# Kernel tuning notes

Measured on AMD Instinct MI355X. Metric: run time of the kernel, lower is better.

The kernel has to match this reference:

```python
import jax, jax.numpy as jnp
import numpy as np

B, T, U = 8, 200, 50
D_ENC, D_DEC, D_FUSION, VOCAB = 512, 512, 640, 1024


def setup_inputs() -> dict:
    key = jax.random.key(0)
    ks = jax.random.split(key, 11)
    s = lambda d: 1.0 / np.sqrt(d)
    return {
        "encoder_out": jax.random.normal(ks[0], (B, T, D_ENC), jnp.float32),
        "decoder_out": jax.random.normal(ks[1], (B, U, D_DEC), jnp.float32),
        "ot_decoder_feature": jax.random.normal(ks[2], (B, T, D_DEC), jnp.float32),
        "W_enc": jax.random.uniform(ks[3], (D_ENC, D_FUSION), jnp.float32, -s(D_ENC), s(D_ENC)),
        "b_enc": jax.random.uniform(ks[4], (D_FUSION,), jnp.float32, -s(D_ENC), s(D_ENC)),
        "W_ot": jax.random.uniform(ks[5], (D_DEC, D_FUSION), jnp.float32, -s(D_DEC), s(D_DEC)),
        "b_ot": jax.random.uniform(ks[6], (D_FUSION,), jnp.float32, -s(D_DEC), s(D_DEC)),
        "W_dec": jax.random.uniform(ks[7], (D_DEC, D_FUSION), jnp.float32, -s(D_DEC), s(D_DEC)),
        "b_dec": jax.random.uniform(ks[8], (D_FUSION,), jnp.float32, -s(D_DEC), s(D_DEC)),
        "W_out": jax.random.uniform(ks[9], (D_FUSION, VOCAB), jnp.float32, -s(D_FUSION), s(D_FUSION)),
        "b_out": jax.random.uniform(ks[10], (VOCAB,), jnp.float32, -s(D_FUSION), s(D_FUSION)),
    }


def reference(encoder_out, decoder_out, ot_decoder_feature,
              W_enc, b_enc, W_ot, b_ot, W_dec, b_dec, W_out, b_out):
    # proj_enc + proj_ot_dec: both [B, T, d_fusion]
    fused = (jnp.einsum('bte,ef->btf', encoder_out, W_enc) + b_enc
             + jnp.einsum('btd,df->btf', ot_decoder_feature, W_ot) + b_ot)
    proj_dec = jnp.einsum('bud,df->buf', decoder_out, W_dec) + b_dec  # [B, U, d_fusion]
    # broadcast add over T x U, tanh, then final projection to vocab
    joint = jnp.tanh(fused[:, :, None, :] + proj_dec[:, None, :, :])  # [B, T, U, d_fusion]
    logits = jnp.einsum('btuf,fv->btuv', joint, W_out) + b_out  # [B, T, U, vocab]
    return logits
```

## Files before the change

### kernel.cpp

```cpp
#include <hip/hip_runtime.h>
#include <math.h>

typedef __bf16 bf16_t;
typedef __bf16 bf16x8 __attribute__((ext_vector_type(8)));
typedef float f32x4 __attribute__((ext_vector_type(4)));
typedef int i32x4 __attribute__((ext_vector_type(4)));
typedef int i32x2 __attribute__((ext_vector_type(2)));

#define SW_SCALE 0.03952847075f

#define GLOAD_LDS16(g, l)                                                      \
  __builtin_amdgcn_global_load_lds(                                            \
      (const __attribute__((address_space(1))) void*)(g),                      \
      (__attribute__((address_space(3))) void*)(l), 16, 0, 0)

__global__ __launch_bounds__(256) void prep_kernel(
    const float* __restrict__ enc, const float* __restrict__ dec,
    const float* __restrict__ ot, const float* __restrict__ W_enc,
    const float* __restrict__ W_ot, const float* __restrict__ W_dec,
    const float* __restrict__ W_out, bf16_t* __restrict__ Acat,
    bf16_t* __restrict__ Dec, bf16_t* __restrict__ WcatT,
    bf16_t* __restrict__ WdecT, signed char* __restrict__ WoutT8) {
  __shared__ float T[32][33];
  const int tid = threadIdx.x;
  const int b = blockIdx.x;

  if (b < 900) {
    const int idx8 = (b * 256 + tid) * 8;
    const int N0 = 1600 * 1024;
    if (idx8 < N0) {
      const int r = idx8 >> 10, c = idx8 & 1023;
      const float* src = (c < 512) ? enc + (r << 9) + c : ot + (r << 9) + c - 512;
      f32x4 v0 = *(const f32x4*)src;
      f32x4 v1 = *(const f32x4*)(src + 4);
      bf16x8 o;
#pragma unroll
      for (int e = 0; e < 4; ++e) {
        o[e] = (bf16_t)v0[e];
        o[e + 4] = (bf16_t)v1[e];
      }
      *(bf16x8*)(Acat + idx8) = o;
    } else {
      const int j = idx8 - N0;
      if (j < 400 * 512) {
        f32x4 v0 = *(const f32x4*)(dec + j);
        f32x4 v1 = *(const f32x4*)(dec + j + 4);
        bf16x8 o;
#pragma unroll
        for (int e = 0; e < 4; ++e) {
          o[e] = (bf16_t)v0[e];
          o[e + 4] = (bf16_t)v1[e];
        }
        *(bf16x8*)(Dec + j) = o;
      }
    }
    return;
  }

  const int tx = tid & 31, ty = tid >> 5;
  if (b < 1540) {
    const int b2 = b - 900;
    const int kt = b2 / 20, ft = b2 - kt * 20;
    const int k0 = kt * 32, f0 = ft * 32;
#pragma unroll
    for (int j = 0; j < 4; ++j) {
      const int kk = k0 + ty + j * 8;
      T[ty + j * 8][tx] = (kk < 512) ? W_enc[kk * 640 + f0 + tx]
                                     : W_ot[(kk - 512) * 640 + f0 + tx];
    }
    __syncthreads();
#pragma unroll
    for (int j = 0; j < 4; ++j) {
      const int ff = f0 + ty + j * 8;
      WcatT[ff * 1024 + k0 + tx] = (bf16_t)T[tx][ty + j * 8];
    }
    return;
  }
  if (b < 1860) {
    const int b2 = b - 1540;
    const int kt = b2 / 20, ft = b2 - kt * 20;
    const int k0 = kt * 32, f0 = ft * 32;
#pragma unroll
    for (int j = 0; j < 4; ++j)
      T[ty + j * 8][tx] = W_dec[(k0 + ty + j * 8) * 640 + f0 + tx];
    __syncthreads();
#pragma unroll
    for (int j = 0; j < 4; ++j) {
      const int ff = f0 + ty + j * 8;
      WdecT[ff * 512 + k0 + tx] = (bf16_t)T[tx][ty + j * 8];
    }
    return;
  }
  {
    const int b2 = b - 1860;
    const int vt = b2 / 20, ft = b2 - vt * 20;
    const int v0 = vt * 32, f0 = ft * 32;
#pragma unroll
    for (int j = 0; j < 4; ++j)
      T[ty + j * 8][tx] = W_out[(f0 + ty + j * 8) * 1024 + v0 + tx];
    __syncthreads();
#pragma unroll
    for (int j = 0; j < 4; ++j) {
      const int vv = v0 + ty + j * 8;
      float w = T[tx][ty + j * 8] * (127.0f / SW_SCALE);
      w = fminf(fmaxf(w, -127.0f), 127.0f);
      WoutT8[(size_t)vv * 640 + f0 + tx] = (signed char)__float2int_rn(w);
    }
  }
}

__global__ __launch_bounds__(256) void gemm_tanh_kernel(
    const bf16_t* __restrict__ A, const bf16_t* __restrict__ Bt,
    const float* __restrict__ bias1, const float* __restrict__ bias2,
    float* __restrict__ out, int M, int K) {
  __shared__ __align__(16) unsigned char L[2][16384];
  const int tid = threadIdx.x;
  const int wid = tid >> 6, l = tid & 63;
  const int wm = wid >> 1, wn = wid & 1;
  const int r0 = blockIdx.y * 64, n0 = blockIdx.x * 64;

  const int sperm = ((l & 3) ^ ((l >> 3) & 3)) * 8;
  int ra0 = r0 + wm * 32 + (l >> 2);
  if (ra0 > M - 1) ra0 = M - 1;
  int ra1 = r0 + wm * 32 + 16 + (l >> 2);
  if (ra1 > M - 1) ra1 = M - 1;
  const bf16_t* gA0 = A + (size_t)ra0 * K + sperm;
  const bf16_t* gA1 = A + (size_t)ra1 * K + sperm;
  const bf16_t* gB0 = Bt + (size_t)(n0 + wn * 32 + (l >> 2)) * K + sperm;
  const bf16_t* gB1 = gB0 + (size_t)16 * K;
  const int wb = wid * 4096;

  const int lr = l & 15, kg = l >> 4;
  const int swz = (kg ^ ((lr >> 1) & 3)) << 4;
  const int aO = wb + lr * 64 + swz;
  const int bO = wb + 2048 + lr * 64 + swz;

#define ST1_STAGE(t, buf)                                                      \
  {                                                                            \
    GLOAD_LDS16(gA0 + (t) * 32, L[buf] + wb);                                  \
    GLOAD_LDS16(gA1 + (t) * 32, L[buf] + wb + 1024);                           \
    GLOAD_LDS16(gB0 + (t) * 32, L[buf] + wb + 2048);                           \
    GLOAD_LDS16(gB1 + (t) * 32, L[buf] + wb + 3072);                           \
  }

  f32x4 acc[2][2] = {};
  const int steps = K >> 5;
  ST1_STAGE(0, 0);
#pragma unroll 1
  for (int ks = 0; ks < steps; ++ks) {
    const int cur = ks & 1, nxt = cur ^ 1;
    if (ks < steps - 1) ST1_STAGE(ks + 1, nxt);
    __builtin_amdgcn_sched_barrier(0);
    if (ks < steps - 1) {
      asm volatile("s_waitcnt vmcnt(4)" ::: "memory");
    } else {
      asm volatile("s_waitcnt vmcnt(0)" ::: "memory");
    }
    __builtin_amdgcn_sched_barrier(0);
    bf16x8 af[2], bfr[2];
#pragma unroll
    for (int a = 0; a < 2; ++a)
      af[a] = *(const bf16x8*)(L[cur] + aO + a * 1024);
#pragma unroll
    for (int b = 0; b < 2; ++b)
      bfr[b] = *(const bf16x8*)(L[cur] + bO + b * 1024);
#pragma unroll
    for (int a = 0; a < 2; ++a)
#pragma unroll
      for (int b = 0; b < 2; ++b)
        acc[a][b] = __builtin_amdgcn_mfma_f32_16x16x32_bf16(af[a], bfr[b],
                                                            acc[a][b], 0, 0, 0);
  }
#undef ST1_STAGE

#pragma unroll
  for (int a = 0; a < 2; ++a)
#pragma unroll
    for (int b = 0; b < 2; ++b) {
      int col = n0 + wn * 32 + b * 16 + lr;
      float bv = bias1[col] + (bias2 ? bias2[col] : 0.0f);
#pragma unroll
      for (int j = 0; j < 4; ++j) {
        int rg = r0 + wm * 32 + a * 16 + kg * 4 + j;
        if (rg < M) out[(size_t)rg * 640 + col] = tanhf(acc[a][b][j] + bv);
      }
    }
}

__global__ __launch_bounds__(256) void materialize8_kernel(
    const float* __restrict__ ta,
    const float* __restrict__ tb,
    signed char* __restrict__ A8) {
  const int idx = blockIdx.x * 256 + threadIdx.x;
  const int row = idx / 80;
  const int c8 = idx - row * 80;
  const int frow = row / 50;
  const int bidx = row / 10000;
  const int u = row - frow * 50;
  const float* tap = ta + (size_t)frow * 640 + c8 * 8;
  const float* tbp = tb + (size_t)(bidx * 50 + u) * 640 + c8 * 8;
  f32x4 xa0 = *(const f32x4*)tap, xa1 = *(const f32x4*)(tap + 4);
  f32x4 xb0 = *(const f32x4*)tbp, xb1 = *(const f32x4*)(tbp + 4);
  int q[8];
#pragma unroll
  for (int e = 0; e < 4; ++e) {
    float d0 = fmaxf(1.0f + xa0[e] * xb0[e], 1e-6f);
    q[e] = __float2int_rn((xa0[e] + xb0[e]) * __builtin_amdgcn_rcpf(d0) * 127.0f);
    float d1 = fmaxf(1.0f + xa1[e] * xb1[e], 1e-6f);
    q[e + 4] =
        __float2int_rn((xa1[e] + xb1[e]) * __builtin_amdgcn_rcpf(d1) * 127.0f);
  }
  i32x2 pk;
  pk[0] = (q[0] & 255) | ((q[1] & 255) << 8) | ((q[2] & 255) << 16) | (q[3] << 24);
  pk[1] = (q[4] & 255) | ((q[5] & 255) << 8) | ((q[6] & 255) << 16) | (q[7] << 24);
  *(i32x2*)(A8 + (size_t)row * 656 + c8 * 8) = pk;
}

__global__ __launch_bounds__(512, 4) void joint_gemm_kernel(
    const signed char* __restrict__ A8,
    const signed char* __restrict__ W8,
    const float* __restrict__ b_out,
    float* __restrict__ out) {
  __shared__ __align__(16) signed char Al[2][21504];
  __shared__ __align__(16) float Tr[8][32 * 20];
  const int tid = threadIdx.x;
  const int w = tid >> 6, l = tid & 63;
  const int lr = l & 15, kg = l >> 4;

  const int orig = blockIdx.x;
  const int mg = (orig & 7) + 8 * (orig >> 6);
  const int strip = (orig >> 3) & 7;
  if (mg >= 313) return;
  const int c0w = strip * 128 + w * 16;

  i32x4 Bf[10];
  const signed char* gW = W8 + (size_t)(c0w + lr) * 640 + kg * 16;
#pragma unroll
  for (int t = 0; t < 10; ++t) Bf[t] = *(const i32x4*)(gW + t * 64);
  const float bv = b_out[c0w + lr];

  const int i0 = w * 3;
  const int ni = (i0 < 21) ? ((i0 + 3 <= 21) ? 3 : 21 - i0) : 0;
  const size_t mbase = (size_t)mg * 256 * 656;

#define JSTAGE(c, buf)                                                         \
  {                                                                            \
    const signed char* s_ = A8 + mbase + (size_t)(c) * (32 * 656);             \
    for (int k_ = 0; k_ < ni; ++k_) {                                          \
      const int i_ = i0 + k_;                                                  \
      const int off_ = (i_ == 20) ? 19968 : i_ * 1024;                         \
      GLOAD_LDS16(s_ + off_ + l * 16, Al[buf] + off_);                         \
    }                                                                          \
  }

  JSTAGE(0, 0);

  const float cfac = SW_SCALE / (127.0f * 127.0f);
  float* trw = Tr[w];

#pragma unroll 1
  for (int c = 0; c < 8; ++c) {
    const int buf = c & 1;
    if (c < 7) JSTAGE(c + 1, buf ^ 1);
    __builtin_amdgcn_sched_barrier(0);
    if (c == 0) {
      asm volatile("s_waitcnt vmcnt(3)" ::: "memory");
    } else if (c < 7) {
      asm volatile("s_waitcnt vmcnt(5)" ::: "memory");
    } else {
      asm volatile("s_waitcnt vmcnt(2)" ::: "memory");
    }
    __builtin_amdgcn_sched_barrier(0);
    __builtin_amdgcn_s_barrier();
    __builtin_amdgcn_sched_barrier(0);

    i32x4 acc0 = {}, acc1 = {};
#pragma unroll
    for (int t = 0; t < 10; ++t) {
      i32x4 a0 = *(const i32x4*)(Al[buf] + lr * 656 + t * 64 + kg * 16);
      i32x4 a1 = *(const i32x4*)(Al[buf] + (16 + lr) * 656 + t * 64 + kg * 16);
      acc0 = __builtin_amdgcn_mfma_i32_16x16x64_i8(a0, Bf[t], acc0, 0, 0, 0);
      acc1 = __builtin_amdgcn_mfma_i32_16x16x64_i8(a1, Bf[t], acc1, 0, 0, 0);
    }

#pragma unroll
    for (int j = 0; j < 4; ++j) {
      trw[(kg * 4 + j) * 20 + lr] = (float)acc0[j] * cfac + bv;
      trw[(16 + kg * 4 + j) * 20 + lr] = (float)acc1[j] * cfac + bv;
    }
    asm volatile("s_waitcnt lgkmcnt(0)" ::: "memory");
    const int part = l & 3;
#pragma unroll
    for (int it = 0; it < 2; ++it) {
      const int row = it * 16 + (l >> 2);
      f32x4 v = *(const f32x4*)(trw + row * 20 + part * 4);
      const int grow = mg * 256 + c * 32 + row;
      if (grow < 80000)
        __builtin_nontemporal_store(
            v, (f32x4*)(out + (size_t)grow * 1024 + c0w + part * 4));
    }
    __builtin_amdgcn_sched_barrier(0);
    __builtin_amdgcn_s_barrier();
  }
#undef JSTAGE
}

extern "C" void kernel_launch(void* const* d_in, const int* in_sizes, int n_in,
                              void* d_out, int out_size, void* d_ws,
                              size_t ws_size, hipStream_t stream) {
  const float* enc = (const float*)d_in[0];
  const float* dec = (const float*)d_in[1];
  const float* ot = (const float*)d_in[2];
  const float* W_enc = (const float*)d_in[3];
  const float* b_enc = (const float*)d_in[4];
  const float* W_ot = (const float*)d_in[5];
  const float* b_ot = (const float*)d_in[6];
  const float* W_dec = (const float*)d_in[7];
  const float* b_dec = (const float*)d_in[8];
  const float* W_out = (const float*)d_in[9];
  const float* b_out = (const float*)d_in[10];
  float* out = (float*)d_out;

  char* ws = (char*)d_ws;
  size_t off = 0;
  auto alloc = [&](size_t bytes) {
    void* p = ws + off;
    off += (bytes + 255) & ~(size_t)255;
    return p;
  };
  float* ta = (float*)alloc(1600 * 640 * 4);
  float* tb = (float*)alloc(400 * 640 * 4);
  bf16_t* Acat = (bf16_t*)alloc(1600 * 1024 * 2);
  bf16_t* Dec = (bf16_t*)alloc(400 * 512 * 2);
  bf16_t* WcatT = (bf16_t*)alloc(640 * 1024 * 2);
  bf16_t* WdecT = (bf16_t*)alloc(640 * 512 * 2);
  signed char* WoutT8 = (signed char*)alloc(1024 * 640);
  signed char* A8 = (signed char*)alloc((size_t)80128 * 656);

  prep_kernel<<<2500, 256, 0, stream>>>(enc, dec, ot, W_enc, W_ot, W_dec,
                                        W_out, Acat, Dec, WcatT, WdecT, WoutT8);
  gemm_tanh_kernel<<<dim3(10, 25), 256, 0, stream>>>(Acat, WcatT, b_enc, b_ot,
                                                     ta, 1600, 1024);
  gemm_tanh_kernel<<<dim3(10, 7), 256, 0, stream>>>(Dec, WdecT, b_dec, nullptr,
                                                    tb, 400, 512);
  materialize8_kernel<<<25000, 256, 0, stream>>>(ta, tb, A8);
  joint_gemm_kernel<<<2560, 512, 0, stream>>>(A8, WoutT8, b_out, out);
}
```

Measured before the change: 142.8 us.

## Merge stage-1 GEMMs into one launch, triple-buffer loads, halve joint GEMM M-tiles

The two projection GEMMs now run in a single launch, with block rows selecting which problem each block handles. This removes one kernel launch and lets the small decoder GEMM overlap with the large one. The stage-1 K loop moves from double to triple buffering with a prefetch distance of two, at the cost of more LDS. The joint GEMM now processes 128 rows per block instead of 256, doubling the grid and remapping block indices, and the row bounds guard on stores is dropped. Each block now reloads its W_out fragments for half as much work, and partial-wave behaviour and L2 locality change.

```diff
diff --git a/kernel.cpp b/kernel.cpp
--- a/kernel.cpp
+++ b/kernel.cpp
@@ -109,15 +109,27 @@
   }
 }
 
-__global__ __launch_bounds__(256) void gemm_tanh_kernel(
-    const bf16_t* __restrict__ A, const bf16_t* __restrict__ Bt,
-    const float* __restrict__ bias1, const float* __restrict__ bias2,
-    float* __restrict__ out, int M, int K) {
-  __shared__ __align__(16) unsigned char L[2][16384];
+__global__ __launch_bounds__(256) void stage1_kernel(
+    const bf16_t* __restrict__ Acat, const bf16_t* __restrict__ WcatT,
+    const float* __restrict__ b_enc, const float* __restrict__ b_ot,
+    float* __restrict__ ta, const bf16_t* __restrict__ Dec,
+    const bf16_t* __restrict__ WdecT, const float* __restrict__ b_dec,
+    float* __restrict__ tb) {
+  __shared__ __align__(16) unsigned char L[3][16384];
   const int tid = threadIdx.x;
   const int wid = tid >> 6, l = tid & 63;
   const int wm = wid >> 1, wn = wid & 1;
-  const int r0 = blockIdx.y * 64, n0 = blockIdx.x * 64;
+
+  const bool big = (blockIdx.y < 25);
+  const int M = big ? 1600 : 400;
+  const int K = big ? 1024 : 512;
+  const bf16_t* A = big ? Acat : Dec;
+  const bf16_t* Bt = big ? WcatT : WdecT;
+  const float* bias1 = big ? b_enc : b_dec;
+  const float* bias2 = big ? b_ot : nullptr;
+  float* out = big ? ta : tb;
+  const int r0 = (big ? blockIdx.y : blockIdx.y - 25) * 64;
+  const int n0 = blockIdx.x * 64;
 
   const int sperm = ((l & 3) ^ ((l >> 3) & 3)) * 8;
   int ra0 = r0 + wm * 32 + (l >> 2);
@@ -135,23 +147,26 @@
   const int aO = wb + lr * 64 + swz;
   const int bO = wb + 2048 + lr * 64 + swz;
 
-#define ST1_STAGE(t, buf)                                                      \
+#define ST1_STAGE(t, s)                                                        \
   {                                                                            \
-    GLOAD_LDS16(gA0 + (t) * 32, L[buf] + wb);                                  \
-    GLOAD_LDS16(gA1 + (t) * 32, L[buf] + wb + 1024);                           \
-    GLOAD_LDS16(gB0 + (t) * 32, L[buf] + wb + 2048);                           \
-    GLOAD_LDS16(gB1 + (t) * 32, L[buf] + wb + 3072);                           \
+    GLOAD_LDS16(gA0 + (t) * 32, L[s] + wb);                                    \
+    GLOAD_LDS16(gA1 + (t) * 32, L[s] + wb + 1024);                             \
+    GLOAD_LDS16(gB0 + (t) * 32, L[s] + wb + 2048);                             \
+    GLOAD_LDS16(gB1 + (t) * 32, L[s] + wb + 3072);                             \
   }
 
   f32x4 acc[2][2] = {};
   const int steps = K >> 5;
   ST1_STAGE(0, 0);
+  ST1_STAGE(1, 1);
 #pragma unroll 1
   for (int ks = 0; ks < steps; ++ks) {
-    const int cur = ks & 1, nxt = cur ^ 1;
-    if (ks < steps - 1) ST1_STAGE(ks + 1, nxt);
-    __builtin_amdgcn_sched_barrier(0);
-    if (ks < steps - 1) {
+    const int cur = ks % 3;
+    if (ks < steps - 2) {
+      ST1_STAGE(ks + 2, (ks + 2) % 3);
+      __builtin_amdgcn_sched_barrier(0);
+      asm volatile("s_waitcnt vmcnt(8)" ::: "memory");
+    } else if (ks == steps - 2) {
       asm volatile("s_waitcnt vmcnt(4)" ::: "memory");
     } else {
       asm volatile("s_waitcnt vmcnt(0)" ::: "memory");
@@ -228,9 +243,9 @@
   const int lr = l & 15, kg = l >> 4;
 
   const int orig = blockIdx.x;
-  const int mg = (orig & 7) + 8 * (orig >> 6);
+  const int mg = (orig & 7) * 80 + (orig >> 6);
   const int strip = (orig >> 3) & 7;
-  if (mg >= 313) return;
+  if (mg >= 625) return;
   const int c0w = strip * 128 + w * 16;
 
   i32x4 Bf[10];
@@ -241,7 +256,7 @@
 
   const int i0 = w * 3;
   const int ni = (i0 < 21) ? ((i0 + 3 <= 21) ? 3 : 21 - i0) : 0;
-  const size_t mbase = (size_t)mg * 256 * 656;
+  const size_t mbase = (size_t)mg * 128 * 656;
 
 #define JSTAGE(c, buf)                                                         \
   {                                                                            \
@@ -259,13 +274,13 @@
   float* trw = Tr[w];
 
 #pragma unroll 1
-  for (int c = 0; c < 8; ++c) {
+  for (int c = 0; c < 4; ++c) {
     const int buf = c & 1;
-    if (c < 7) JSTAGE(c + 1, buf ^ 1);
+    if (c < 3) JSTAGE(c + 1, buf ^ 1);
     __builtin_amdgcn_sched_barrier(0);
     if (c == 0) {
       asm volatile("s_waitcnt vmcnt(3)" ::: "memory");
-    } else if (c < 7) {
+    } else if (c < 3) {
       asm volatile("s_waitcnt vmcnt(5)" ::: "memory");
     } else {
       asm volatile("s_waitcnt vmcnt(2)" ::: "memory");
@@ -294,10 +309,9 @@
     for (int it = 0; it < 2; ++it) {
       const int row = it * 16 + (l >> 2);
       f32x4 v = *(const f32x4*)(trw + row * 20 + part * 4);
-      const int grow = mg * 256 + c * 32 + row;
-      if (grow < 80000)
-        __builtin_nontemporal_store(
-            v, (f32x4*)(out + (size_t)grow * 1024 + c0w + part * 4));
+      const int grow = mg * 128 + c * 32 + row;
+      __builtin_nontemporal_store(
+          v, (f32x4*)(out + (size_t)grow * 1024 + c0w + part * 4));
     }
     __builtin_amdgcn_sched_barrier(0);
     __builtin_amdgcn_s_barrier();
@@ -339,10 +353,8 @@
 
   prep_kernel<<<2500, 256, 0, stream>>>(enc, dec, ot, W_enc, W_ot, W_dec,
                                         W_out, Acat, Dec, WcatT, WdecT, WoutT8);
-  gemm_tanh_kernel<<<dim3(10, 25), 256, 0, stream>>>(Acat, WcatT, b_enc, b_ot,
-                                                     ta, 1600, 1024);
-  gemm_tanh_kernel<<<dim3(10, 7), 256, 0, stream>>>(Dec, WdecT, b_dec, nullptr,
-                                                    tb, 400, 512);
+  stage1_kernel<<<dim3(10, 32), 256, 0, stream>>>(Acat, WcatT, b_enc, b_ot, ta,
+                                                  Dec, WdecT, b_dec, tb);
   materialize8_kernel<<<25000, 256, 0, stream>>>(ta, tb, A8);
-  joint_gemm_kernel<<<2560, 512, 0, stream>>>(A8, WoutT8, b_out, out);
-}
+  joint_gemm_kernel<<<5120, 512, 0, stream>>>(A8, WoutT8, b_out, out);
+}
```

Result: slower. 147.8 us (+3.5%).
